# Performance work log

Hardware: AMD Instinct MI355X
Metric: run time of the kernel (lower is better)

The kernel has to match this reference:

```python
import jax, jax.numpy as jnp
import numpy as np

EPS = 1e-7  # keras.backend.epsilon()
NUM_ROUTING = 3


def squash(v, axis=-1):
    s2 = jnp.sum(jnp.square(v), axis=axis, keepdims=True)
    scale = s2 / (1.0 + s2) / jnp.sqrt(s2 + EPS)
    return scale * v


def setup_inputs() -> dict:
    key = jax.random.key(0)
    k1, k2 = jax.random.split(key)
    B, N_in, C, d_in, d_out = 64, 4096, 10, 8, 16
    x = jax.random.normal(k1, (B, N_in, d_in), dtype=jnp.float32)
    # glorot-ish scale for transformation weights [N_in, C, d_in, d_out]
    W = jax.random.normal(k2, (N_in, C, d_in, d_out), dtype=jnp.float32) * (1.0 / np.sqrt(d_in + d_out))
    return {"x": x, "W": W}


def reference(x, W):
    # u_hat[b,n,c,e] = sum_d x[b,n,d] * W[n,c,d,e]  -- the tile+multiply+reduce in the original
    u_hat = jnp.einsum('bnd,ncde->bnce', x, W)  # [B, N_in, C, d_out]
    B, N_in, C, _ = u_hat.shape
    b = jnp.zeros((B, N_in, C), dtype=u_hat.dtype)
    v = None
    for i in range(NUM_ROUTING):
        c = jax.nn.softmax(b, axis=2)                    # [B, N_in, C]
        s = jnp.einsum('bnc,bnce->bce', c, u_hat)        # [B, C, d_out]
        v = squash(s)                                    # [B, C, d_out]
        if i < NUM_ROUTING - 1:
            agreement = jnp.einsum('bnce,bce->bnc', u_hat, v)
            b = b + agreement
    return v
```

## Files before the change

### kernel.cpp

```cpp
#include <hip/hip_runtime.h>
#include <hip/hip_fp16.h>

#define B_ 64
#define N_ 4096
#define C_ 10
#define D_ 8
#define E_ 16
#define EPS_ 1e-7f
#define NT_ 4
#define NBLK_ (N_ / NT_)
#define NSLOT_ NBLK_
#define PROW_ 80

typedef _Float16 h2_t __attribute__((ext_vector_type(2)));
typedef __fp16   p2_t __attribute__((ext_vector_type(2)));

__device__ inline unsigned pkh(float a, float b) {
    p2_t t = __builtin_amdgcn_cvt_pkrtz(a, b);
    return *(unsigned*)&t;
}
#if __has_builtin(__builtin_amdgcn_fdot2)
__device__ inline float fd2(unsigned a, unsigned b, float c) {
    h2_t av = *(h2_t*)&a, bv = *(h2_t*)&b;
    return __builtin_amdgcn_fdot2(av, bv, c, false);
}
#else
__device__ inline float fd2(unsigned a, unsigned b, float c) {
    h2_t av = *(h2_t*)&a, bv = *(h2_t*)&b;
    return fmaf((float)av.x, (float)bv.x, fmaf((float)av.y, (float)bv.y, c));
}
#endif
__device__ inline float hlo(unsigned u) { h2_t t = *(h2_t*)&u; return (float)t.x; }
__device__ inline float hhi(unsigned u) { h2_t t = *(h2_t*)&u; return (float)t.y; }
__device__ inline unsigned hpack(float a, float b) {
    __half2 t = __floats2half2_rn(a, b);
    return *(unsigned*)&t;
}
__device__ inline float2 hunpack(unsigned u) {
    return __half22float2(*(const __half2*)&u);
}

template <bool UNIFORM>
__global__ __launch_bounds__(256, 3) void caps_pass(
    const float* __restrict__ x, const float* __restrict__ W,
    const float* __restrict__ v_cum, unsigned* __restrict__ partial)
{
    __shared__ uint4    wlds[NT_ * C_ * 16];
    __shared__ unsigned xlds[NT_ * B_ * 4];
    __shared__ float    xch[2][2][2][16][2];

    const int tid = (int)threadIdx.x;
    const int blk = (int)blockIdx.x;
    const int n0  = blk * NT_;

    {
        const float4* wg = (const float4*)W + (size_t)blk * (NT_ * 320);
#pragma unroll
        for (int k = 0; k < 3; ++k) {
            const int g = k * 256 + tid;
            if (g < NT_ * C_ * 16) {
                const int n   = g / 160;
                const int rem = g - n * 160;
                const int c   = rem >> 4;
                const int r2  = rem & 15;
                const int d2  = r2 >> 2;
                const int eqs = r2 & 3;
                const float4 g0 = wg[n * 320 + c * 32 + (2 * d2) * 4 + eqs];
                const float4 g1 = wg[n * 320 + c * 32 + (2 * d2 + 1) * 4 + eqs];
                wlds[((n * C_ + c) * 4 + d2) * 4 + eqs] =
                    make_uint4(pkh(g0.x, g1.x), pkh(g0.y, g1.y),
                               pkh(g0.z, g1.z), pkh(g0.w, g1.w));
            }
        }
    }
    {
        const float4* xg = (const float4*)x;
#pragma unroll
        for (int k = 0; k < 2; ++k) {
            const int g = k * 256 + tid;
            const int b = g >> 3;
            const int r = g & 7;
            const int n = r >> 1;
            const int dq = r & 1;
            const float4 v = xg[((size_t)b * N_ + n0 + n) * 2 + dq];
            *(uint2*)&xlds[(n * B_ + b) * 4 + dq * 2] =
                make_uint2(pkh(v.x, v.y), pkh(v.z, v.w));
        }
    }
    __syncthreads();

    const int wv   = tid >> 6;
    const int lane = tid & 63;
    const int eq   = lane & 3;
    const int bl   = lane >> 2;
    const int h    = wv & 1;
    const int cg   = wv >> 1;
    const int b0   = h * 32 + bl;
    const int b1   = b0 + 16;
    const int cbase = cg * 5;

    unsigned vcp0[5][2], vcp1[5][2];
    if (!UNIFORM) {
#pragma unroll
        for (int cc = 0; cc < 5; ++cc) {
            const int c = cbase + cc;
            const float4 a = *(const float4*)(v_cum + (b0 * C_ + c) * E_ + eq * 4);
            vcp0[cc][0] = pkh(a.x, a.y); vcp0[cc][1] = pkh(a.z, a.w);
            const float4 d = *(const float4*)(v_cum + (b1 * C_ + c) * E_ + eq * 4);
            vcp1[cc][0] = pkh(d.x, d.y); vcp1[cc][1] = pkh(d.z, d.w);
        }
    }

    float4 acc0[5], acc1[5];
#pragma unroll
    for (int cc = 0; cc < 5; ++cc) {
        acc0[cc] = make_float4(0.f, 0.f, 0.f, 0.f);
        acc1[cc] = make_float4(0.f, 0.f, 0.f, 0.f);
    }

#pragma unroll 1
    for (int j = 0; j < NT_; ++j) {
        const uint4 xq0 = *(const uint4*)&xlds[(j * B_ + b0) * 4];
        const uint4 xq1 = *(const uint4*)&xlds[(j * B_ + b1) * 4];
        const unsigned xa[4] = {xq0.x, xq0.y, xq0.z, xq0.w};
        const unsigned xb[4] = {xq1.x, xq1.y, xq1.z, xq1.w};

        if (UNIFORM) {
#pragma unroll
            for (int cc = 0; cc < 5; ++cc) {
                const uint4* wq = &wlds[(j * C_ + cbase + cc) * 16];
#pragma unroll
                for (int d2 = 0; d2 < 4; ++d2) {
                    const uint4 q = wq[d2 * 4 + eq];
                    acc0[cc].x = fd2(xa[d2], q.x, acc0[cc].x);
                    acc0[cc].y = fd2(xa[d2], q.y, acc0[cc].y);
                    acc0[cc].z = fd2(xa[d2], q.z, acc0[cc].z);
                    acc0[cc].w = fd2(xa[d2], q.w, acc0[cc].w);
                    acc1[cc].x = fd2(xb[d2], q.x, acc1[cc].x);
                    acc1[cc].y = fd2(xb[d2], q.y, acc1[cc].y);
                    acc1[cc].z = fd2(xb[d2], q.z, acc1[cc].z);
                    acc1[cc].w = fd2(xb[d2], q.w, acc1[cc].w);
                }
            }
        } else {
            unsigned uhp0[5][2], uhp1[5][2];
            float wgt0[5], wgt1[5];
            float s0 = 0.f, s1 = 0.f;
#pragma unroll
            for (int cc = 0; cc < 5; ++cc) {
                const uint4* wq = &wlds[(j * C_ + cbase + cc) * 16];
                float4 u0 = make_float4(0.f, 0.f, 0.f, 0.f);
                float4 u1 = make_float4(0.f, 0.f, 0.f, 0.f);
#pragma unroll
                for (int d2 = 0; d2 < 4; ++d2) {
                    const uint4 q = wq[d2 * 4 + eq];
                    u0.x = fd2(xa[d2], q.x, u0.x);
                    u0.y = fd2(xa[d2], q.y, u0.y);
                    u0.z = fd2(xa[d2], q.z, u0.z);
                    u0.w = fd2(xa[d2], q.w, u0.w);
                    u1.x = fd2(xb[d2], q.x, u1.x);
                    u1.y = fd2(xb[d2], q.y, u1.y);
                    u1.z = fd2(xb[d2], q.z, u1.z);
                    u1.w = fd2(xb[d2], q.w, u1.w);
                }
                const unsigned up00 = pkh(u0.x, u0.y), up01 = pkh(u0.z, u0.w);
                const unsigned up10 = pkh(u1.x, u1.y), up11 = pkh(u1.z, u1.w);
                float t0 = fd2(up00, vcp0[cc][0], fd2(up01, vcp0[cc][1], 0.f));
                t0 += __shfl_xor(t0, 1); t0 += __shfl_xor(t0, 2);
                float t1 = fd2(up10, vcp1[cc][0], fd2(up11, vcp1[cc][1], 0.f));
                t1 += __shfl_xor(t1, 1); t1 += __shfl_xor(t1, 2);
                wgt0[cc] = __expf(t0); s0 += wgt0[cc];
                wgt1[cc] = __expf(t1); s1 += wgt1[cc];
                uhp0[cc][0] = up00; uhp0[cc][1] = up01;
                uhp1[cc][0] = up10; uhp1[cc][1] = up11;
            }
            if (eq == 0) {
                xch[j & 1][cg][h][bl][0] = s0;
                xch[j & 1][cg][h][bl][1] = s1;
            }
            __syncthreads();
            const float i0 = 1.f / (s0 + xch[j & 1][cg ^ 1][h][bl][0]);
            const float i1 = 1.f / (s1 + xch[j & 1][cg ^ 1][h][bl][1]);
#pragma unroll
            for (int cc = 0; cc < 5; ++cc) {
                const float g0 = wgt0[cc] * i0, g1 = wgt1[cc] * i1;
                acc0[cc].x = fmaf(g0, hlo(uhp0[cc][0]), acc0[cc].x);
                acc0[cc].y = fmaf(g0, hhi(uhp0[cc][0]), acc0[cc].y);
                acc0[cc].z = fmaf(g0, hlo(uhp0[cc][1]), acc0[cc].z);
                acc0[cc].w = fmaf(g0, hhi(uhp0[cc][1]), acc0[cc].w);
                acc1[cc].x = fmaf(g1, hlo(uhp1[cc][0]), acc1[cc].x);
                acc1[cc].y = fmaf(g1, hhi(uhp1[cc][0]), acc1[cc].y);
                acc1[cc].z = fmaf(g1, hlo(uhp1[cc][1]), acc1[cc].z);
                acc1[cc].w = fmaf(g1, hhi(uhp1[cc][1]), acc1[cc].w);
            }
        }
    }

    const float fold = UNIFORM ? 0.1f : 1.f;
#pragma unroll
    for (int cc = 0; cc < 5; ++cc) {
        const int c = cbase + cc;
        *(uint2*)(partial + ((size_t)b0 * NSLOT_ + blk) * PROW_ + c * 8 + eq * 2) =
            make_uint2(hpack(acc0[cc].x * fold, acc0[cc].y * fold),
                       hpack(acc0[cc].z * fold, acc0[cc].w * fold));
        *(uint2*)(partial + ((size_t)b1 * NSLOT_ + blk) * PROW_ + c * 8 + eq * 2) =
            make_uint2(hpack(acc1[cc].x * fold, acc1[cc].y * fold),
                       hpack(acc1[cc].z * fold, acc1[cc].w * fold));
    }
}

__global__ __launch_bounds__(512) void caps_reduce(
    const unsigned* __restrict__ partial, float* __restrict__ v_cum,
    float* __restrict__ out, int mode)
{
    const int b = (int)blockIdx.x;
    const int tid = (int)threadIdx.x;
    __shared__ float4 red[8][40];
    const int gh  = tid >> 6;
    const int col = tid & 63;
    if (col < 40) {
        const unsigned* base =
            partial + ((size_t)b * NSLOT_ + (size_t)gh * (NSLOT_ / 8)) * PROW_ + col * 2;
        float s0 = 0.f, s1 = 0.f, s2 = 0.f, s3 = 0.f;
        for (int k = 0; k < NSLOT_ / 8; ++k) {
            const uint2 u = *(const uint2*)(base + (size_t)k * PROW_);
            const float2 f0 = hunpack(u.x);
            const float2 f1 = hunpack(u.y);
            s0 += f0.x; s1 += f0.y; s2 += f1.x; s3 += f1.y;
        }
        red[gh][col] = make_float4(s0, s1, s2, s3);
    }
    __syncthreads();
    if (tid < C_ * E_) {
        const int c4 = tid >> 2, e4 = tid & 3;
        float s = 0.f;
#pragma unroll
        for (int g = 0; g < 8; ++g) s += ((const float*)&red[g][c4])[e4];
        float p = s * s;
        p += __shfl_xor(p, 1); p += __shfl_xor(p, 2);
        p += __shfl_xor(p, 4); p += __shfl_xor(p, 8);
        const float sc = (p / (1.f + p)) * rsqrtf(p + EPS_);
        const float v = sc * s;
        const int o = b * (C_ * E_) + tid;
        if (mode == 2)      out[o] = v;
        else if (mode == 0) v_cum[o] = v;
        else                v_cum[o] += v;
    }
}

extern "C" void kernel_launch(void* const* d_in, const int* in_sizes, int n_in,
                              void* d_out, int out_size, void* d_ws, size_t ws_size,
                              hipStream_t stream) {
    const float* x = (const float*)d_in[0];
    const float* W = (const float*)d_in[1];
    float* out = (float*)d_out;

    unsigned* partial = (unsigned*)d_ws;
    float* v_cum = (float*)((char*)d_ws +
        (size_t)B_ * NSLOT_ * PROW_ * sizeof(unsigned));

    for (int t = 0; t < 3; ++t) {
        if (t == 0)
            caps_pass<true ><<<dim3(NBLK_), 256, 0, stream>>>(x, W, v_cum, partial);
        else
            caps_pass<false><<<dim3(NBLK_), 256, 0, stream>>>(x, W, v_cum, partial);
        caps_reduce<<<dim3(B_), 512, 0, stream>>>(partial, v_cum, out, t);
    }
}
```

Baseline: 90.61 us.

## Split partial reduction into two-stage kernels and raise pass occupancy hint

Replaces the single 64-block reduce kernel with a two-stage reduction. The first stage uses 512 blocks, each reading a slice of slots with 16-byte loads and writing float sub-sums. A small second stage then sums the 8 sub-groups and applies squash. The goal is to spread the ~21MB partial-buffer read across many more CUs than 64 blocks could use. The change also raises caps_pass launch bounds min-blocks from 3 to 4, which may constrain registers and cause spills, and it adds an extra kernel launch per routing iteration.

```diff
diff --git a/kernel.cpp b/kernel.cpp
--- a/kernel.cpp
+++ b/kernel.cpp
@@ -11,6 +11,7 @@
 #define NBLK_ (N_ / NT_)
 #define NSLOT_ NBLK_
 #define PROW_ 80
+#define NSG_ 8
 
 typedef _Float16 h2_t __attribute__((ext_vector_type(2)));
 typedef __fp16   p2_t __attribute__((ext_vector_type(2)));
@@ -41,7 +42,7 @@
 }
 
 template <bool UNIFORM>
-__global__ __launch_bounds__(256, 3) void caps_pass(
+__global__ __launch_bounds__(256, 4) void caps_pass(
     const float* __restrict__ x, const float* __restrict__ W,
     const float* __restrict__ v_cum, unsigned* __restrict__ partial)
 {
@@ -209,43 +210,63 @@
     }
 }
 
-__global__ __launch_bounds__(512) void caps_reduce(
-    const unsigned* __restrict__ partial, float* __restrict__ v_cum,
+__global__ __launch_bounds__(256) void caps_redA(
+    const unsigned* __restrict__ partial, float* __restrict__ sub)
+{
+    const int b  = (int)blockIdx.x >> 3;
+    const int sg = (int)blockIdx.x & 7;
+    const int tid = (int)threadIdx.x;
+    const int sc   = tid >> 5;
+    const int col4 = tid & 31;
+    __shared__ float red[8][20][8];
+    if (col4 < 20) {
+        float s[8];
+#pragma unroll
+        for (int p = 0; p < 8; ++p) s[p] = 0.f;
+        const int slot0 = sg * (NSLOT_ / NSG_) + sc * 16;
+        const uint4* base = (const uint4*)(partial +
+            ((size_t)b * NSLOT_ + slot0) * PROW_) + col4;
+#pragma unroll 4
+        for (int k = 0; k < 16; ++k) {
+            const uint4 q = base[k * (PROW_ / 4)];
+            const float2 f0 = hunpack(q.x), f1 = hunpack(q.y);
+            const float2 f2 = hunpack(q.z), f3 = hunpack(q.w);
+            s[0] += f0.x; s[1] += f0.y; s[2] += f1.x; s[3] += f1.y;
+            s[4] += f2.x; s[5] += f2.y; s[6] += f3.x; s[7] += f3.y;
+        }
+#pragma unroll
+        for (int p = 0; p < 8; ++p) red[sc][col4][p] = s[p];
+    }
+    __syncthreads();
+    if (tid < 160) {
+        const int c4 = tid >> 3, p = tid & 7;
+        float s = 0.f;
+#pragma unroll
+        for (int ch = 0; ch < 8; ++ch) s += red[ch][c4][p];
+        sub[((size_t)b * NSG_ + sg) * (C_ * E_) + c4 * 8 + p] = s;
+    }
+}
+
+__global__ __launch_bounds__(192) void caps_redB(
+    const float* __restrict__ sub, float* __restrict__ v_cum,
     float* __restrict__ out, int mode)
 {
     const int b = (int)blockIdx.x;
     const int tid = (int)threadIdx.x;
-    __shared__ float4 red[8][40];
-    const int gh  = tid >> 6;
-    const int col = tid & 63;
-    if (col < 40) {
-        const unsigned* base =
-            partial + ((size_t)b * NSLOT_ + (size_t)gh * (NSLOT_ / 8)) * PROW_ + col * 2;
-        float s0 = 0.f, s1 = 0.f, s2 = 0.f, s3 = 0.f;
-        for (int k = 0; k < NSLOT_ / 8; ++k) {
-            const uint2 u = *(const uint2*)(base + (size_t)k * PROW_);
-            const float2 f0 = hunpack(u.x);
-            const float2 f1 = hunpack(u.y);
-            s0 += f0.x; s1 += f0.y; s2 += f1.x; s3 += f1.y;
-        }
-        red[gh][col] = make_float4(s0, s1, s2, s3);
-    }
-    __syncthreads();
-    if (tid < C_ * E_) {
-        const int c4 = tid >> 2, e4 = tid & 3;
-        float s = 0.f;
-#pragma unroll
-        for (int g = 0; g < 8; ++g) s += ((const float*)&red[g][c4])[e4];
-        float p = s * s;
-        p += __shfl_xor(p, 1); p += __shfl_xor(p, 2);
-        p += __shfl_xor(p, 4); p += __shfl_xor(p, 8);
-        const float sc = (p / (1.f + p)) * rsqrtf(p + EPS_);
-        const float v = sc * s;
-        const int o = b * (C_ * E_) + tid;
-        if (mode == 2)      out[o] = v;
-        else if (mode == 0) v_cum[o] = v;
-        else                v_cum[o] += v;
-    }
+    if (tid >= C_ * E_) return;
+    float s = 0.f;
+#pragma unroll
+    for (int sg = 0; sg < NSG_; ++sg)
+        s += sub[((size_t)b * NSG_ + sg) * (C_ * E_) + tid];
+    float p = s * s;
+    p += __shfl_xor(p, 1); p += __shfl_xor(p, 2);
+    p += __shfl_xor(p, 4); p += __shfl_xor(p, 8);
+    const float sc = (p / (1.f + p)) * rsqrtf(p + EPS_);
+    const float v = sc * s;
+    const int o = b * (C_ * E_) + tid;
+    if (mode == 2)      out[o] = v;
+    else if (mode == 0) v_cum[o] = v;
+    else                v_cum[o] += v;
 }
 
 extern "C" void kernel_launch(void* const* d_in, const int* in_sizes, int n_in,
@@ -256,14 +277,16 @@
     float* out = (float*)d_out;
 
     unsigned* partial = (unsigned*)d_ws;
-    float* v_cum = (float*)((char*)d_ws +
+    float* sub = (float*)((char*)d_ws +
         (size_t)B_ * NSLOT_ * PROW_ * sizeof(unsigned));
+    float* v_cum = sub + (size_t)B_ * NSG_ * C_ * E_;
 
     for (int t = 0; t < 3; ++t) {
         if (t == 0)
             caps_pass<true ><<<dim3(NBLK_), 256, 0, stream>>>(x, W, v_cum, partial);
         else
             caps_pass<false><<<dim3(NBLK_), 256, 0, stream>>>(x, W, v_cum, partial);
-        caps_reduce<<<dim3(B_), 512, 0, stream>>>(partial, v_cum, out, t);
-    }
-}
+        caps_redA<<<dim3(B_ * NSG_), 256, 0, stream>>>(partial, sub);
+        caps_redB<<<dim3(B_), 192, 0, stream>>>(sub, v_cum, out, t);
+    }
+}
```

Measured after the change: 83.77 us. 7.6% less time.
